# Kernel tuning notes

Measured on AMD Instinct MI355X. Metric: run time of the kernel, lower is better.

## Reference

```python
import jax, jax.numpy as jnp
import numpy as np

NUM_NODES = 50000
NUM_EDGES = 800000
INPUT_DIM = 256
OUTPUT_DIM = 256
NUM_HEADS = 8
HEAD_DIM = OUTPUT_DIM // NUM_HEADS


def setup_inputs() -> dict:
    key = jax.random.key(0)
    ks = jax.random.split(key, 14)
    x = jax.random.normal(ks[0], (NUM_NODES, INPUT_DIM), dtype=jnp.float32)
    edge_index = jax.random.randint(ks[1], (2, NUM_EDGES), 0, NUM_NODES, dtype=jnp.int32)
    # timestamps in seconds over ~11.5 days so log1p(|dt|/3600) is informative
    edge_time = jax.random.uniform(ks[2], (NUM_EDGES,), dtype=jnp.float32) * 1e6
    node_time = jax.random.uniform(ks[3], (NUM_NODES,), dtype=jnp.float32) * 1e6
    s_in = 1.0 / np.sqrt(INPUT_DIM)
    s_out = 1.0 / np.sqrt(OUTPUT_DIM)
    s_t = 1.0 / np.sqrt(2.0)
    Wq = jax.random.uniform(ks[4], (INPUT_DIM, OUTPUT_DIM), jnp.float32, -s_in, s_in)
    bq = jax.random.uniform(ks[5], (OUTPUT_DIM,), jnp.float32, -s_in, s_in)
    Wk = jax.random.uniform(ks[6], (INPUT_DIM, OUTPUT_DIM), jnp.float32, -s_in, s_in)
    bk = jax.random.uniform(ks[7], (OUTPUT_DIM,), jnp.float32, -s_in, s_in)
    Wv = jax.random.uniform(ks[8], (INPUT_DIM, OUTPUT_DIM), jnp.float32, -s_in, s_in)
    bv = jax.random.uniform(ks[9], (OUTPUT_DIM,), jnp.float32, -s_in, s_in)
    Wt = jax.random.uniform(ks[10], (2, NUM_HEADS), jnp.float32, -s_t, s_t)
    bt = jax.random.uniform(ks[11], (NUM_HEADS,), jnp.float32, -s_t, s_t)
    Wo = jax.random.uniform(ks[12], (OUTPUT_DIM, OUTPUT_DIM), jnp.float32, -s_out, s_out)
    bo = jax.random.uniform(ks[13], (OUTPUT_DIM,), jnp.float32, -s_out, s_out)
    return {"x": x, "edge_index": edge_index, "edge_time": edge_time, "node_time": node_time,
            "Wq": Wq, "bq": bq, "Wk": Wk, "bk": bk, "Wv": Wv, "bv": bv,
            "Wt": Wt, "bt": bt, "Wo": Wo, "bo": bo}


def reference(x, edge_index, edge_time, node_time, Wq, bq, Wk, bk, Wv, bv, Wt, bt, Wo, bo):
    n = x.shape[0]
    q = (x @ Wq + bq).reshape(n, NUM_HEADS, HEAD_DIM)
    k = (x @ Wk + bk).reshape(n, NUM_HEADS, HEAD_DIM)
    v = (x @ Wv + bv).reshape(n, NUM_HEADS, HEAD_DIM)
    src, dst = edge_index[0], edge_index[1]
    # temporal features per edge
    time_diff = edge_time - node_time[dst]
    time_features = jnp.stack(
        [jnp.sign(time_diff), jnp.log1p(jnp.abs(time_diff) / 3600.0)], axis=-1)  # [E, 2]
    temporal_weights = time_features @ Wt + bt  # [E, H]
    scale = HEAD_DIM ** -0.5
    scores = jnp.einsum('ehd,ehd->eh', q[dst], k[src]) * scale + temporal_weights  # [E, H]
    # softmax over ALL edges per head (dim=0), as in the original
    alpha = jax.nn.softmax(scores, axis=0)  # [E, H]
    msg = alpha[..., None] * v[src]  # [E, H, D]
    out = jax.ops.segment_sum(msg, dst, num_segments=n)  # [N, H, D]
    out = out.reshape(n, OUTPUT_DIM)
    return out @ Wo + bo
```

## Files before the change

### kernel.cpp

```cpp
#include <hip/hip_runtime.h>
#include <hip/hip_bf16.h>

#define NUM_NODES 50000
#define NUM_EDGES 800000
#define NUM_HEADS 8
#define HEAD_DIM 32
#define SCAN_BLOCKS 49
#define NCHUNK32 1563

typedef unsigned short ushort8 __attribute__((ext_vector_type(8)));
typedef float f32x4 __attribute__((ext_vector_type(4)));
typedef __bf16 bf16x8 __attribute__((ext_vector_type(8)));

union BF8 { ushort8 u; bf16x8 b; };

__device__ __forceinline__ unsigned float_to_key(float f) {
    int i = __float_as_int(f);
    return (i >= 0) ? ((unsigned)i | 0x80000000u) : ~(unsigned)i;
}
__device__ __forceinline__ float key_to_float(unsigned u) {
    unsigned b = (u & 0x80000000u) ? (u & 0x7fffffffu) : ~u;
    return __int_as_float((int)b);
}
__device__ __forceinline__ float bf2f(unsigned short u) {
    return __uint_as_float(((unsigned)u) << 16);
}
__device__ __forceinline__ unsigned short f2bf(float f) {
    unsigned u = __float_as_uint(f);
    unsigned r = (u + 0x7fffu + ((u >> 16) & 1u)) >> 16;
    return (unsigned short)r;
}

__global__ __launch_bounds__(256) void deg_kernel(const int* __restrict__ dst_idx, int* __restrict__ deg) {
    int e = blockIdx.x * 256 + threadIdx.x;
    if (e < NUM_EDGES) atomicAdd(&deg[dst_idx[e]], 1);
}

__global__ __launch_bounds__(1024) void scanA_kernel(
    const int* __restrict__ deg, int* __restrict__ offs, int* __restrict__ blocksum)
{
    __shared__ int buf[1024];
    int tid = threadIdx.x;
    int i = blockIdx.x * 1024 + tid;
    int v = (i < NUM_NODES) ? deg[i] : 0;
    buf[tid] = v;
    __syncthreads();
    for (int off = 1; off < 1024; off <<= 1) {
        int t = (tid >= off) ? buf[tid - off] : 0;
        __syncthreads();
        buf[tid] += t;
        __syncthreads();
    }
    if (i < NUM_NODES) offs[i] = buf[tid] - v;
    if (tid == 1023) blocksum[blockIdx.x] = buf[1023];
}

__global__ __launch_bounds__(64) void scanB_kernel(
    const int* __restrict__ blocksum, int* __restrict__ carry, int* __restrict__ offs)
{
    if (threadIdx.x == 0) {
        int acc = 0;
        for (int b = 0; b < SCAN_BLOCKS; b++) { carry[b] = acc; acc += blocksum[b]; }
        offs[NUM_NODES] = acc;
    }
}

__global__ __launch_bounds__(256) void scanC_kernel(
    int* __restrict__ offs, const int* __restrict__ carry, int* __restrict__ cursor)
{
    int i = blockIdx.x * 256 + threadIdx.x;
    if (i < NUM_NODES) {
        int v = offs[i] + carry[i >> 10];
        offs[i] = v;
        cursor[i] = v;
    }
}

__global__ __launch_bounds__(256) void fill2_kernel(
    const int* __restrict__ src_idx, const int* __restrict__ dst_idx,
    const float* __restrict__ edge_time, int* __restrict__ cursor,
    int* __restrict__ src_s, int* __restrict__ dst_s, float* __restrict__ et_s)
{
    int e = blockIdx.x * 256 + threadIdx.x;
    if (e < NUM_EDGES) {
        int d = dst_idx[e];
        int pos = atomicAdd(&cursor[d], 1);
        src_s[pos] = src_idx[e];
        dst_s[pos] = d;
        et_s[pos] = edge_time[e];
    }
}

__global__ __launch_bounds__(256) void wtrans_kernel(
    const float* __restrict__ Wq, const float* __restrict__ Wk,
    const float* __restrict__ Wv, const float* __restrict__ Wo,
    unsigned short* __restrict__ Wt)
{
    __shared__ float t[64][65];
    int nb = blockIdx.x * 64;
    int kb = blockIdx.y * 64;
    int g = nb >> 8;
    const float* W = (g == 0) ? Wq : (g == 1) ? Wk : (g == 2) ? Wv : Wo;
    int n0 = nb & 255;
    int tx = threadIdx.x & 63;
    int ty = threadIdx.x >> 6;
#pragma unroll
    for (int i = 0; i < 16; i++) {
        int k = i * 4 + ty;
        t[tx][k] = W[(size_t)(kb + k) * 256 + n0 + tx];
    }
    __syncthreads();
#pragma unroll
    for (int i = 0; i < 16; i++) {
        int n = i * 4 + ty;
        Wt[(size_t)(nb + n) * 256 + kb + tx] = f2bf(t[n][tx]);
    }
}

__global__ __launch_bounds__(256) void wpack_kernel(
    const unsigned short* __restrict__ Wt, unsigned short* __restrict__ Wpk)
{
    int gid = blockIdx.x * 256 + threadIdx.x;
    int lane = gid & 63;
    int fragidx = gid >> 6;
    int c2 = fragidx & 7;
    int nf = (fragidx >> 3) & 3;
    int cb = (fragidx >> 5) & 3;
    int g = fragidx >> 7;
    int l16 = lane & 15;
    int kg = lane >> 4;
    int n_col = g * 256 + cb * 64 + nf * 16 + l16;
    int k0 = c2 * 32 + kg * 8;
    ushort8 v = *(const ushort8*)(Wt + (size_t)n_col * 256 + k0);
    *(ushort8*)(Wpk + (size_t)gid * 8) = v;
}

__global__ __launch_bounds__(256) void gemm_qkv_mfma6(
    const float* __restrict__ A, int M,
    const unsigned short* __restrict__ Wpk,
    const float* __restrict__ b0, const float* __restrict__ b1, const float* __restrict__ b2,
    unsigned short* __restrict__ O0, unsigned short* __restrict__ O1, unsigned short* __restrict__ O2)
{
    __shared__ unsigned short As[64 * 256];
    int tid = threadIdx.x;
    int rowbase = blockIdx.x * 64;

    {
        int rsub = tid >> 6;
        int c4 = (tid & 63) * 4;
        int cchunk = (tid & 63) >> 1;
        int sub = (tid & 1);
#pragma unroll
        for (int it = 0; it < 16; it++) {
            int row = it * 4 + rsub;
            int grow = rowbase + row;
            float4 av = make_float4(0.f, 0.f, 0.f, 0.f);
            if (grow < M) av = *(const float4*)(A + (size_t)grow * 256 + c4);
            ushort4 o;
            o.x = f2bf(av.x); o.y = f2bf(av.y); o.z = f2bf(av.z); o.w = f2bf(av.w);
            unsigned byte = row * 512 + ((unsigned)(cchunk ^ (row & 7)) << 4) + sub * 8;
            *(ushort4*)((char*)As + byte) = o;
        }
    }
    __syncthreads();

    int lane = tid & 63;
    int wid = tid >> 6;
    int l16 = lane & 15;
    int kg = lane >> 4;

#pragma unroll
    for (int p = 0; p < 3; p++) {
        const float* bias = (p == 0) ? b0 : (p == 1) ? b1 : b2;
        unsigned short* O = (p == 0) ? O0 : (p == 1) ? O1 : O2;

        f32x4 acc[4][4];
#pragma unroll
        for (int m = 0; m < 4; m++)
#pragma unroll
            for (int n = 0; n < 4; n++) acc[m][n] = (f32x4)(0.0f);

        const ushort8* wbase = (const ushort8*)(Wpk + ((size_t)(p * 4 + wid) * 2048 + lane) * 8);

#pragma unroll
        for (int c2 = 0; c2 < 8; c2++) {
            bf16x8 wfr[4];
#pragma unroll
            for (int n = 0; n < 4; n++) {
                BF8 t; t.u = wbase[(n * 8 + c2) * 64];
                wfr[n] = t.b;
            }
            bf16x8 afr[4];
#pragma unroll
            for (int m = 0; m < 4; m++) {
                int row = m * 16 + l16;
                int cchunk = (c2 * 4 + kg) ^ (row & 7);
                BF8 t;
                t.u = *(const ushort8*)((const char*)As + row * 512 + (cchunk << 4));
                afr[m] = t.b;
            }
#pragma unroll
            for (int m = 0; m < 4; m++)
#pragma unroll
                for (int n = 0; n < 4; n++)
                    acc[m][n] = __builtin_amdgcn_mfma_f32_16x16x32_bf16(wfr[n], afr[m], acc[m][n], 0, 0, 0);
        }

#pragma unroll
        for (int m = 0; m < 4; m++) {
            int node = rowbase + m * 16 + l16;
            if (node >= M) continue;
#pragma unroll
            for (int n = 0; n < 4; n++) {
                int lc = wid * 64 + n * 16 + kg * 4;
                float4 bv = *(const float4*)(bias + lc);
                ushort4 o;
                o.x = f2bf(acc[m][n][0] + bv.x);
                o.y = f2bf(acc[m][n][1] + bv.y);
                o.z = f2bf(acc[m][n][2] + bv.z);
                o.w = f2bf(acc[m][n][3] + bv.w);
                int hh = lc >> 5, dd = lc & 31;
                *(ushort4*)(O + ((size_t)hh * NUM_NODES + node) * 32 + dd) = o;
            }
        }
    }
}

__global__ __launch_bounds__(256) void gemm_out_mfma6(
    const unsigned short* __restrict__ aggb, int M,
    const unsigned short* __restrict__ Wpk,
    const float* __restrict__ bias, const float* __restrict__ kscale,
    float* __restrict__ C)
{
    __shared__ unsigned short As[64 * 256];
    int tid = threadIdx.x;
    int rowbase = blockIdx.x * 64;

    {
        int rsub = tid >> 6;
        int c4 = (tid & 63) * 4;
        int cchunk = (tid & 63) >> 1;
        int sub = (tid & 1);
        int hh = c4 >> 5, dd = c4 & 31;
        float ks = kscale[hh];
#pragma unroll
        for (int it = 0; it < 16; it++) {
            int row = it * 4 + rsub;
            int grow = rowbase + row;
            ushort4 av = make_ushort4(0, 0, 0, 0);
            if (grow < M) av = *(const ushort4*)(aggb + ((size_t)hh * NUM_NODES + grow) * 32 + dd);
            ushort4 o;
            o.x = f2bf(bf2f(av.x) * ks); o.y = f2bf(bf2f(av.y) * ks);
            o.z = f2bf(bf2f(av.z) * ks); o.w = f2bf(bf2f(av.w) * ks);
            unsigned byte = row * 512 + ((unsigned)(cchunk ^ (row & 7)) << 4) + sub * 8;
            *(ushort4*)((char*)As + byte) = o;
        }
    }
    __syncthreads();

    int lane = tid & 63;
    int wid = tid >> 6;
    int l16 = lane & 15;
    int kg = lane >> 4;

    f32x4 acc[4][4];
#pragma unroll
    for (int m = 0; m < 4; m++)
#pragma unroll
        for (int n = 0; n < 4; n++) acc[m][n] = (f32x4)(0.0f);

    const ushort8* wbase = (const ushort8*)(Wpk + ((size_t)wid * 2048 + lane) * 8);

#pragma unroll
    for (int c2 = 0; c2 < 8; c2++) {
        bf16x8 wfr[4];
#pragma unroll
        for (int n = 0; n < 4; n++) {
            BF8 t; t.u = wbase[(n * 8 + c2) * 64];
            wfr[n] = t.b;
        }
        bf16x8 afr[4];
#pragma unroll
        for (int m = 0; m < 4; m++) {
            int row = m * 16 + l16;
            int cchunk = (c2 * 4 + kg) ^ (row & 7);
            BF8 t;
            t.u = *(const ushort8*)((const char*)As + row * 512 + (cchunk << 4));
            afr[m] = t.b;
        }
#pragma unroll
        for (int m = 0; m < 4; m++)
#pragma unroll
            for (int n = 0; n < 4; n++)
                acc[m][n] = __builtin_amdgcn_mfma_f32_16x16x32_bf16(wfr[n], afr[m], acc[m][n], 0, 0, 0);
    }

#pragma unroll
    for (int m = 0; m < 4; m++) {
        int node = rowbase + m * 16 + l16;
        if (node >= M) continue;
#pragma unroll
        for (int n = 0; n < 4; n++) {
            int col = wid * 64 + n * 16 + kg * 4;
            float4 bv = *(const float4*)(bias + col);
            float4 o;
            o.x = acc[m][n][0] + bv.x;
            o.y = acc[m][n][1] + bv.y;
            o.z = acc[m][n][2] + bv.z;
            o.w = acc[m][n][3] + bv.w;
            *(float4*)(C + (size_t)node * 256 + col) = o;
        }
    }
}

__global__ __launch_bounds__(256) void score3_kernel(
    const unsigned short* __restrict__ qh, const unsigned short* __restrict__ kh,
    const int* __restrict__ src_s, const int* __restrict__ dst_s,
    const float* __restrict__ et_s, const float* __restrict__ node_time,
    const float* __restrict__ Wt, const float* __restrict__ bt,
    float* __restrict__ scores, unsigned* __restrict__ partialmax)
{
    __shared__ unsigned sm;
    int tid = threadIdx.x;
    if (tid == 0) sm = 0u;
    __syncthreads();
    int h = blockIdx.x & 7;
    int blk = blockIdx.x >> 3;
    float wt0 = Wt[h], wt1 = Wt[8 + h], btv = bt[h];
    const unsigned short* qhh = qh + (size_t)h * NUM_NODES * 32;
    const unsigned short* khh = kh + (size_t)h * NUM_NODES * 32;
    float* sc_h = scores + (size_t)h * NUM_EDGES;
    unsigned mykey = 0u;
    for (int pos = blk * 256 + tid; pos < NUM_EDGES; pos += 128 * 256) {
        int s = src_s[pos], d = dst_s[pos];
        const ushort8* qp = (const ushort8*)(qhh + (size_t)d * 32);
        const ushort8* kp = (const ushort8*)(khh + (size_t)s * 32);
        float dotv = 0.f;
#pragma unroll
        for (int i = 0; i < 4; i++) {
            ushort8 a = qp[i], b = kp[i];
#pragma unroll
            for (int j = 0; j < 8; j++) dotv += bf2f(a[j]) * bf2f(b[j]);
        }
        float td = et_s[pos] - node_time[d];
        float tf0 = (td > 0.f) ? 1.f : ((td < 0.f) ? -1.f : 0.f);
        float tf1 = log1pf(fabsf(td) * (1.f / 3600.f));
        float sc = dotv * 0.17677669529663687f + (tf0 * wt0 + tf1 * wt1 + btv);
        sc_h[pos] = sc;
        unsigned kkey = float_to_key(sc);
        mykey = (kkey > mykey) ? kkey : mykey;
    }
#pragma unroll
    for (int off = 32; off > 0; off >>= 1) {
        unsigned o = __shfl_xor(mykey, off, 64);
        mykey = (o > mykey) ? o : mykey;
    }
    if ((tid & 63) == 0) atomicMax(&sm, mykey);
    __syncthreads();
    if (tid == 0) partialmax[blockIdx.x] = sm;
}

__global__ __launch_bounds__(256) void reduce_max2_kernel(
    const unsigned* __restrict__ partialmax, float* __restrict__ headmax)
{
    int tid = threadIdx.x;
    int h = tid >> 5, lane = tid & 31;
    unsigned m = 0u;
#pragma unroll
    for (int k = 0; k < 4; k++) {
        unsigned v = partialmax[(lane + 32 * k) * 8 + h];
        m = (v > m) ? v : m;
    }
    for (int off = 16; off > 0; off >>= 1) {
        unsigned o = __shfl_down(m, off, 32);
        m = (o > m) ? o : m;
    }
    if (lane == 0) headmax[h] = key_to_float(m);
}

__global__ __launch_bounds__(256) void aggregate7_kernel(
    const unsigned short* __restrict__ vh, const float* __restrict__ scores,
    const int* __restrict__ src_s, const int* __restrict__ offs,
    const float* __restrict__ headmax, unsigned short* __restrict__ aggb,
    float* __restrict__ psum_part)
{
    __shared__ int sSrc[512];
    __shared__ float sP[512];
    __shared__ float blocksum;
    int tid = threadIdx.x;
    int h = blockIdx.x & 7;
    int chunk = blockIdx.x >> 3;
    int nodebase = chunk * 32;
    int g = tid >> 3;
    int ln = tid & 7;
    int node = nodebase + g;
    float m = headmax[h];
    const float* sc_h = scores + (size_t)h * NUM_EDGES;
    const unsigned short* vhh = vh + (size_t)h * NUM_NODES * 32;
    if (tid == 0) blocksum = 0.f;

    int blkstart = offs[nodebase];
    int blkend = offs[(nodebase + 32 < NUM_NODES) ? (nodebase + 32) : NUM_NODES];
    int start = 0, end = 0;
    if (node < NUM_NODES) { start = offs[node]; end = offs[node + 1]; }

    f32x4 a0 = (f32x4)(0.f), a1 = (f32x4)(0.f);
    float ps = 0.f;

    for (int t0 = blkstart; t0 < blkend; t0 += 512) {
        int cnt = min(512, blkend - t0);
        __syncthreads();
        for (int i = tid; i < cnt; i += 256) {
            sSrc[i] = src_s[t0 + i];
            float p = __expf(sc_h[t0 + i] - m);
            sP[i] = p;
            ps += p;
        }
        __syncthreads();
        int lo = (start > t0) ? start : t0;
        int hi = (end < t0 + cnt) ? end : (t0 + cnt);
        int cb = lo;
        for (; cb + 2 <= hi; cb += 2) {
            int i0 = cb - t0;
            int s0 = sSrc[i0], s1 = sSrc[i0 + 1];
            float p0 = sP[i0], p1 = sP[i0 + 1];
            ushort4 v0 = *(const ushort4*)(vhh + (size_t)s0 * 32 + ln * 4);
            ushort4 v1 = *(const ushort4*)(vhh + (size_t)s1 * 32 + ln * 4);
            a0[0] += p0 * bf2f(v0.x); a0[1] += p0 * bf2f(v0.y);
            a0[2] += p0 * bf2f(v0.z); a0[3] += p0 * bf2f(v0.w);
            a1[0] += p1 * bf2f(v1.x); a1[1] += p1 * bf2f(v1.y);
            a1[2] += p1 * bf2f(v1.z); a1[3] += p1 * bf2f(v1.w);
        }
        if (cb < hi) {
            int i0 = cb - t0;
            int s0 = sSrc[i0];
            float p0 = sP[i0];
            ushort4 v0 = *(const ushort4*)(vhh + (size_t)s0 * 32 + ln * 4);
            a0[0] += p0 * bf2f(v0.x); a0[1] += p0 * bf2f(v0.y);
            a0[2] += p0 * bf2f(v0.z); a0[3] += p0 * bf2f(v0.w);
        }
    }

    if (node < NUM_NODES) {
        ushort4 o;
        o.x = f2bf(a0[0] + a1[0]); o.y = f2bf(a0[1] + a1[1]);
        o.z = f2bf(a0[2] + a1[2]); o.w = f2bf(a0[3] + a1[3]);
        *(ushort4*)(aggb + ((size_t)h * NUM_NODES + node) * 32 + ln * 4) = o;
    }

    __syncthreads();
#pragma unroll
    for (int off = 32; off > 0; off >>= 1) ps += __shfl_xor(ps, off, 64);
    if ((tid & 63) == 0) atomicAdd(&blocksum, ps);
    __syncthreads();
    if (tid == 0) psum_part[blockIdx.x] = blocksum;
}

__global__ __launch_bounds__(256) void reduce_psum2_kernel(
    const float* __restrict__ psum_part, float* __restrict__ headinv)
{
    int tid = threadIdx.x;
    int h = tid >> 5, lane = tid & 31;
    float s = 0.f;
    for (int i = lane; i < NCHUNK32; i += 32) s += psum_part[i * 8 + h];
    for (int off = 16; off > 0; off >>= 1) s += __shfl_down(s, off, 32);
    if (lane == 0) headinv[h] = 1.f / s;
}

extern "C" void kernel_launch(void* const* d_in, const int* in_sizes, int n_in,
                              void* d_out, int out_size, void* d_ws, size_t ws_size,
                              hipStream_t stream) {
    const float* x = (const float*)d_in[0];
    const int* ei = (const int*)d_in[1];
    const int* src_idx = ei;
    const int* dst_idx = ei + NUM_EDGES;
    const float* edge_time = (const float*)d_in[2];
    const float* node_time = (const float*)d_in[3];
    const float* Wq = (const float*)d_in[4];  const float* bq = (const float*)d_in[5];
    const float* Wk = (const float*)d_in[6];  const float* bk = (const float*)d_in[7];
    const float* Wv = (const float*)d_in[8];  const float* bv = (const float*)d_in[9];
    const float* Wt = (const float*)d_in[10]; const float* bt = (const float*)d_in[11];
    const float* Wo = (const float*)d_in[12]; const float* bo = (const float*)d_in[13];
    float* out = (float*)d_out;

    char* w = (char*)d_ws;
    unsigned short* qb = (unsigned short*)w; w += (size_t)NUM_NODES * 256 * 2;
    unsigned short* kb = (unsigned short*)w; w += (size_t)NUM_NODES * 256 * 2;
    unsigned short* vb = (unsigned short*)w; w += (size_t)NUM_NODES * 256 * 2;
    float* scores = (float*)w;      w += (size_t)NUM_EDGES * 8 * 4;
    unsigned short* aggb = (unsigned short*)w; w += (size_t)NUM_NODES * 256 * 2;
    int* src_s = (int*)w;           w += (size_t)NUM_EDGES * 4;
    int* dst_s = (int*)w;           w += (size_t)NUM_EDGES * 4;
    float* et_s = (float*)w;        w += (size_t)NUM_EDGES * 4;
    int* deg = (int*)w;             w += (size_t)NUM_NODES * 4;
    int* offs = (int*)w;            w += (size_t)(NUM_NODES + 1) * 4;
    int* cursor = (int*)w;          w += (size_t)NUM_NODES * 4;
    unsigned* partialmax = (unsigned*)w; w += 1024 * 4;
    float* psum_part = (float*)w;   w += (size_t)NCHUNK32 * 8 * 4;
    float* headmax = (float*)w;     w += 8 * 4;
    float* headinv = (float*)w;     w += 8 * 4;
    int* blocksum = (int*)w;        w += 64 * 4;
    int* bcarry = (int*)w;          w += 64 * 4;
    unsigned short* Wtb = (unsigned short*)w; w += (size_t)1024 * 256 * 2;
    unsigned short* Wpk = (unsigned short*)w; w += (size_t)1024 * 256 * 2;

    hipMemsetAsync(deg, 0, (size_t)NUM_NODES * 4, stream);

    dim3 gw(16, 4);
    wtrans_kernel<<<gw, 256, 0, stream>>>(Wq, Wk, Wv, Wo, Wtb);
    wpack_kernel<<<128, 256, 0, stream>>>(Wtb, Wpk);

    deg_kernel<<<(NUM_EDGES + 255) / 256, 256, 0, stream>>>(dst_idx, deg);
    scanA_kernel<<<SCAN_BLOCKS, 1024, 0, stream>>>(deg, offs, blocksum);
    scanB_kernel<<<1, 64, 0, stream>>>(blocksum, bcarry, offs);
    scanC_kernel<<<(NUM_NODES + 255) / 256, 256, 0, stream>>>(offs, bcarry, cursor);
    fill2_kernel<<<(NUM_EDGES + 255) / 256, 256, 0, stream>>>(src_idx, dst_idx, edge_time,
                                                              cursor, src_s, dst_s, et_s);

    gemm_qkv_mfma6<<<(NUM_NODES + 63) / 64, 256, 0, stream>>>(
        x, NUM_NODES, Wpk, bq, bk, bv, qb, kb, vb);

    score3_kernel<<<1024, 256, 0, stream>>>(qb, kb, src_s, dst_s, et_s, node_time,
                                            Wt, bt, scores, partialmax);
    reduce_max2_kernel<<<1, 256, 0, stream>>>(partialmax, headmax);

    aggregate7_kernel<<<NCHUNK32 * 8, 256, 0, stream>>>(
        vb, scores, src_s, offs, headmax, aggb, psum_part);
    reduce_psum2_kernel<<<1, 256, 0, stream>>>(psum_part, headinv);

    gemm_out_mfma6<<<(NUM_NODES + 63) / 64, 256, 0, stream>>>(
        aggb, NUM_NODES, Wpk + (size_t)768 * 256, bo, headinv, out);
}
```

Measured before the change: 331.4 us.

## Precompute temporal features in fill, store Q/K as fp16, use fdot2 in scoring

Moves the sign/log1p temporal feature computation from the per-head score kernel into the edge-sort fill kernel, so it is computed once per edge instead of once per head. Source and destination indices are packed into int2 for a single load. Q and K are now written as fp16 so the score dot product can use packed fdot2 instructions. The score grid is doubled and the max reduction is widened to match. This trades extra fill-stage writes and fp16 range and precision risk for fewer transcendental and ALU operations in scoring.

```diff
diff --git a/kernel.cpp b/kernel.cpp
--- a/kernel.cpp
+++ b/kernel.cpp
@@ -11,8 +11,19 @@
 typedef unsigned short ushort8 __attribute__((ext_vector_type(8)));
 typedef float f32x4 __attribute__((ext_vector_type(4)));
 typedef __bf16 bf16x8 __attribute__((ext_vector_type(8)));
+typedef _Float16 h2 __attribute__((ext_vector_type(2)));
 
 union BF8 { ushort8 u; bf16x8 b; };
+union H8 { ushort8 u; h2 h[4]; };
+
+#if defined(__has_builtin)
+#if __has_builtin(__builtin_amdgcn_fdot2)
+#define FDOT2(a, b, c) __builtin_amdgcn_fdot2((a), (b), (c), false)
+#endif
+#endif
+#ifndef FDOT2
+#define FDOT2(a, b, c) ((float)(a)[0] * (float)(b)[0] + (float)(a)[1] * (float)(b)[1] + (c))
+#endif
 
 __device__ __forceinline__ unsigned float_to_key(float f) {
     int i = __float_as_int(f);
@@ -29,6 +40,10 @@
     unsigned u = __float_as_uint(f);
     unsigned r = (u + 0x7fffu + ((u >> 16) & 1u)) >> 16;
     return (unsigned short)r;
+}
+__device__ __forceinline__ unsigned short f2h(float f) {
+    _Float16 h = (_Float16)f;
+    return *(unsigned short*)&h;
 }
 
 __global__ __launch_bounds__(256) void deg_kernel(const int* __restrict__ dst_idx, int* __restrict__ deg) {
@@ -76,18 +91,24 @@
     }
 }
 
-__global__ __launch_bounds__(256) void fill2_kernel(
+__global__ __launch_bounds__(256) void fill3_kernel(
     const int* __restrict__ src_idx, const int* __restrict__ dst_idx,
-    const float* __restrict__ edge_time, int* __restrict__ cursor,
-    int* __restrict__ src_s, int* __restrict__ dst_s, float* __restrict__ et_s)
+    const float* __restrict__ edge_time, const float* __restrict__ node_time,
+    int* __restrict__ cursor, int2* __restrict__ sd, float2* __restrict__ tf,
+    int* __restrict__ src_s)
 {
     int e = blockIdx.x * 256 + threadIdx.x;
     if (e < NUM_EDGES) {
         int d = dst_idx[e];
+        int s = src_idx[e];
         int pos = atomicAdd(&cursor[d], 1);
-        src_s[pos] = src_idx[e];
-        dst_s[pos] = d;
-        et_s[pos] = edge_time[e];
+        int2 v; v.x = s; v.y = d;
+        sd[pos] = v;
+        src_s[pos] = s;
+        float td = edge_time[e] - node_time[d];
+        float t0 = (td > 0.f) ? 1.f : ((td < 0.f) ? -1.f : 0.f);
+        float t1 = log1pf(fabsf(td) * (1.f / 3600.f));
+        tf[pos] = make_float2(t0, t1);
     }
 }
 
@@ -135,7 +156,7 @@
     *(ushort8*)(Wpk + (size_t)gid * 8) = v;
 }
 
-__global__ __launch_bounds__(256) void gemm_qkv_mfma6(
+__global__ __launch_bounds__(256) void gemm_qkv_mfma7(
     const float* __restrict__ A, int M,
     const unsigned short* __restrict__ Wpk,
     const float* __restrict__ b0, const float* __restrict__ b1, const float* __restrict__ b2,
@@ -215,10 +236,17 @@
                 int lc = wid * 64 + n * 16 + kg * 4;
                 float4 bv = *(const float4*)(bias + lc);
                 ushort4 o;
-                o.x = f2bf(acc[m][n][0] + bv.x);
-                o.y = f2bf(acc[m][n][1] + bv.y);
-                o.z = f2bf(acc[m][n][2] + bv.z);
-                o.w = f2bf(acc[m][n][3] + bv.w);
+                if (p < 2) {
+                    o.x = f2h(acc[m][n][0] + bv.x);
+                    o.y = f2h(acc[m][n][1] + bv.y);
+                    o.z = f2h(acc[m][n][2] + bv.z);
+                    o.w = f2h(acc[m][n][3] + bv.w);
+                } else {
+                    o.x = f2bf(acc[m][n][0] + bv.x);
+                    o.y = f2bf(acc[m][n][1] + bv.y);
+                    o.z = f2bf(acc[m][n][2] + bv.z);
+                    o.w = f2bf(acc[m][n][3] + bv.w);
+                }
                 int hh = lc >> 5, dd = lc & 31;
                 *(ushort4*)(O + ((size_t)hh * NUM_NODES + node) * 32 + dd) = o;
             }
@@ -313,10 +341,9 @@
     }
 }
 
-__global__ __launch_bounds__(256) void score3_kernel(
+__global__ __launch_bounds__(256) void score4_kernel(
     const unsigned short* __restrict__ qh, const unsigned short* __restrict__ kh,
-    const int* __restrict__ src_s, const int* __restrict__ dst_s,
-    const float* __restrict__ et_s, const float* __restrict__ node_time,
+    const int2* __restrict__ sd, const float2* __restrict__ tf,
     const float* __restrict__ Wt, const float* __restrict__ bt,
     float* __restrict__ scores, unsigned* __restrict__ partialmax)
 {
@@ -331,21 +358,21 @@
     const unsigned short* khh = kh + (size_t)h * NUM_NODES * 32;
     float* sc_h = scores + (size_t)h * NUM_EDGES;
     unsigned mykey = 0u;
-    for (int pos = blk * 256 + tid; pos < NUM_EDGES; pos += 128 * 256) {
-        int s = src_s[pos], d = dst_s[pos];
-        const ushort8* qp = (const ushort8*)(qhh + (size_t)d * 32);
-        const ushort8* kp = (const ushort8*)(khh + (size_t)s * 32);
+    const int stride = 256 * 256;
+    for (int pos = blk * 256 + tid; pos < NUM_EDGES; pos += stride) {
+        int2 e = sd[pos];
+        float2 t = tf[pos];
+        const ushort8* qp = (const ushort8*)(qhh + (size_t)e.y * 32);
+        const ushort8* kp = (const ushort8*)(khh + (size_t)e.x * 32);
         float dotv = 0.f;
 #pragma unroll
         for (int i = 0; i < 4; i++) {
-            ushort8 a = qp[i], b = kp[i];
-#pragma unroll
-            for (int j = 0; j < 8; j++) dotv += bf2f(a[j]) * bf2f(b[j]);
-        }
-        float td = et_s[pos] - node_time[d];
-        float tf0 = (td > 0.f) ? 1.f : ((td < 0.f) ? -1.f : 0.f);
-        float tf1 = log1pf(fabsf(td) * (1.f / 3600.f));
-        float sc = dotv * 0.17677669529663687f + (tf0 * wt0 + tf1 * wt1 + btv);
+            H8 a, b;
+            a.u = qp[i]; b.u = kp[i];
+#pragma unroll
+            for (int j = 0; j < 4; j++) dotv = FDOT2(a.h[j], b.h[j], dotv);
+        }
+        float sc = dotv * 0.17677669529663687f + (t.x * wt0 + t.y * wt1 + btv);
         sc_h[pos] = sc;
         unsigned kkey = float_to_key(sc);
         mykey = (kkey > mykey) ? kkey : mykey;
@@ -360,15 +387,14 @@
     if (tid == 0) partialmax[blockIdx.x] = sm;
 }
 
-__global__ __launch_bounds__(256) void reduce_max2_kernel(
+__global__ __launch_bounds__(256) void reduce_max3_kernel(
     const unsigned* __restrict__ partialmax, float* __restrict__ headmax)
 {
     int tid = threadIdx.x;
     int h = tid >> 5, lane = tid & 31;
     unsigned m = 0u;
-#pragma unroll
-    for (int k = 0; k < 4; k++) {
-        unsigned v = partialmax[(lane + 32 * k) * 8 + h];
+    for (int i = lane; i < 256; i += 32) {
+        unsigned v = partialmax[i * 8 + h];
         m = (v > m) ? v : m;
     }
     for (int off = 16; off > 0; off >>= 1) {
@@ -489,13 +515,13 @@
     unsigned short* vb = (unsigned short*)w; w += (size_t)NUM_NODES * 256 * 2;
     float* scores = (float*)w;      w += (size_t)NUM_EDGES * 8 * 4;
     unsigned short* aggb = (unsigned short*)w; w += (size_t)NUM_NODES * 256 * 2;
+    int2* sd = (int2*)w;            w += (size_t)NUM_EDGES * 8;
+    float2* tfb = (float2*)w;       w += (size_t)NUM_EDGES * 8;
     int* src_s = (int*)w;           w += (size_t)NUM_EDGES * 4;
-    int* dst_s = (int*)w;           w += (size_t)NUM_EDGES * 4;
-    float* et_s = (float*)w;        w += (size_t)NUM_EDGES * 4;
     int* deg = (int*)w;             w += (size_t)NUM_NODES * 4;
     int* offs = (int*)w;            w += (size_t)(NUM_NODES + 1) * 4;
     int* cursor = (int*)w;          w += (size_t)NUM_NODES * 4;
-    unsigned* partialmax = (unsigned*)w; w += 1024 * 4;
+    unsigned* partialmax = (unsigned*)w; w += 2048 * 4;
     float* psum_part = (float*)w;   w += (size_t)NCHUNK32 * 8 * 4;
     float* headmax = (float*)w;     w += 8 * 4;
     float* headinv = (float*)w;     w += 8 * 4;
@@ -514,15 +540,14 @@
     scanA_kernel<<<SCAN_BLOCKS, 1024, 0, stream>>>(deg, offs, blocksum);
     scanB_kernel<<<1, 64, 0, stream>>>(blocksum, bcarry, offs);
     scanC_kernel<<<(NUM_NODES + 255) / 256, 256, 0, stream>>>(offs, bcarry, cursor);
-    fill2_kernel<<<(NUM_EDGES + 255) / 256, 256, 0, stream>>>(src_idx, dst_idx, edge_time,
-                                                              cursor, src_s, dst_s, et_s);
-
-    gemm_qkv_mfma6<<<(NUM_NODES + 63) / 64, 256, 0, stream>>>(
+    fill3_kernel<<<(NUM_EDGES + 255) / 256, 256, 0, stream>>>(
+        src_idx, dst_idx, edge_time, node_time, cursor, sd, tfb, src_s);
+
+    gemm_qkv_mfma7<<<(NUM_NODES + 63) / 64, 256, 0, stream>>>(
         x, NUM_NODES, Wpk, bq, bk, bv, qb, kb, vb);
 
-    score3_kernel<<<1024, 256, 0, stream>>>(qb, kb, src_s, dst_s, et_s, node_time,
-                                            Wt, bt, scores, partialmax);
-    reduce_max2_kernel<<<1, 256, 0, stream>>>(partialmax, headmax);
+    score4_kernel<<<2048, 256, 0, stream>>>(qb, kb, sd, tfb, Wt, bt, scores, partialmax);
+    reduce_max3_kernel<<<1, 256, 0, stream>>>(partialmax, headmax);
 
     aggregate7_kernel<<<NCHUNK32 * 8, 256, 0, stream>>>(
         vb, scores, src_s, offs, headmax, aggb, psum_part);
```

Measured after the change: 347.2 us. +4.7%, slower.
